# Performance work log

Hardware: AMD Instinct MI355X
Metric: run time of the kernel (lower is better)

## Reference

```python
import jax, jax.numpy as jnp
import numpy as np

N_FILTER = 64
IMAGE_SIZE = 64
CHANNELS = 3
N_CALLS = 16  # n_calls * 16 with n_calls=1
EPS = 1e-5


def _sobel_kernels(c):
    kx = jnp.array([[-1., 0., 1.], [-2., 0., 2.], [-1., 0., 1.]], jnp.float32) / 8.0
    ky = kx.T
    # depthwise OIHW kernels: (C, 1, 3, 3)
    return jnp.tile(kx[None, None], (c, 1, 1, 1)), jnp.tile(ky[None, None], (c, 1, 1, 1))


def _dwconv(x, k):
    return jax.lax.conv_general_dilated(
        x, k, window_strides=(1, 1), padding='SAME',
        feature_group_count=x.shape[1],
        dimension_numbers=('NCHW', 'OIHW', 'NCHW'))


def setup_inputs() -> dict:
    key = jax.random.key(0)
    k1, k2, k3 = jax.random.split(key, 3)
    B, L = 16, 512
    fin, fout = N_FILTER * 3, N_FILTER
    return {
        'lat': jax.random.normal(k1, (B, L), jnp.float32),
        'Wk': jax.random.normal(k2, (L, fin * fout), jnp.float32) * 0.02,
        'bk': jnp.zeros((fin * fout,), jnp.float32),
        'Wb': jax.random.normal(k3, (L, fout), jnp.float32) * 0.02,
        'bb': jnp.zeros((fout,), jnp.float32),
        'leak_factor': jnp.asarray(0.1, jnp.float32),
    }


def reference(lat, Wk, bk, Wb, bb, leak_factor):
    B = lat.shape[0]
    fin, fout = N_FILTER * 3, N_FILTER
    kx, ky = _sobel_kernels(N_FILTER)

    # seed: zeros with a 1.0 in channel 0 at the image center
    out0 = jnp.zeros((B, N_FILTER, IMAGE_SIZE, IMAGE_SIZE), jnp.float32)
    out0 = out0.at[:, 0, IMAGE_SIZE // 2, IMAGE_SIZE // 2].set(1.0)

    leak = jnp.clip(leak_factor, 0.001, 1000.0)

    # per-sample dynamic 1x1 conv weights/bias (constant across the loop)
    w = (lat @ Wk + bk).reshape(B, fout, fin)   # (B, fout, fin)
    b = (lat @ Wb + bb)                          # (B, fout)

    def step(out, _):
        # Sobel perception: [identity, grad_x, grad_y] -> (B, 3*nf, H, W)
        p = jnp.concatenate([out, _dwconv(out, kx), _dwconv(out, ky)], axis=1)
        # InstanceNorm2d (affine=False): normalize over H, W per sample/channel
        mu = p.mean(axis=(2, 3), keepdims=True)
        var = p.var(axis=(2, 3), keepdims=True)
        p = (p - mu) * jax.lax.rsqrt(var + EPS)
        # latent-conditioned dynamic 1x1 conv
        new = jnp.einsum('bchw,boc->bohw', p, w) + b[:, :, None, None]
        out = out + leak * new
        return out, out

    out, embs = jax.lax.scan(step, out0, None, length=N_CALLS)
    out_embs = jnp.concatenate([out0[None], embs], axis=0)  # (N_CALLS+1, B, nf, H, W)

    out_raw = out[:, :CHANNELS]
    return jnp.clip(out_raw, -1.0, 1.0), out_embs, out_raw
```

## Files before the change

### kernel.cpp

```cpp
#include <hip/hip_runtime.h>
#include <cstdint>
#include <cstddef>

#define NB 16
#define NC 64
#define HW 4096
#define SLICE ((size_t)(NB*NC*HW))
#define NSTEP 16

#define WS_WT    ((size_t)0)
#define WS_BV    ((size_t)196608)
#define WS_LATT  ((size_t)197632)
#define WS_SV    ((size_t)205824)
#define WS_SVMU  ((size_t)208896)

typedef _Float16 half8 __attribute__((ext_vector_type(8)));
typedef float f32x4 __attribute__((ext_vector_type(4)));

__global__ void k_latT(const float* __restrict__ lat, float* __restrict__ latT) {
  int t = threadIdx.x;
  for (int idx = t; idx < 16*512; idx += 256) {
    int b = idx >> 9, k = idx & 511;
    latT[k*16 + b] = lat[idx];
  }
}

__global__ __launch_bounds__(256) void k_w(const float* __restrict__ latT,
    const float* __restrict__ Wk, const float* __restrict__ bk,
    const float* __restrict__ Wb, const float* __restrict__ bb,
    float* __restrict__ wT, float* __restrict__ bvec) {
  int t = threadIdx.x;
  if (blockIdx.x < 48) {
    int j = blockIdx.x*256 + t;
    float acc[16];
#pragma unroll
    for (int b = 0; b < 16; b++) acc[b] = 0.f;
#pragma unroll 4
    for (int k = 0; k < 512; k++) {
      float wv = Wk[(size_t)k*12288 + j];
      const float* lt = (const float*)__builtin_assume_aligned(latT + k*16, 64);
#pragma unroll
      for (int b = 0; b < 16; b++) acc[b] = fmaf(lt[b], wv, acc[b]);
    }
    int o = j / 192, cf = j % 192;
    int g = cf >> 6, c = cf & 63;
    float bkj = bk[j];
#pragma unroll
    for (int b = 0; b < 16; b++)
      wT[(((size_t)(b*3 + g))*64 + o)*64 + c] = acc[b] + bkj;
  } else if (t < 64) {
    int j = t;
    float acc[16];
#pragma unroll
    for (int b = 0; b < 16; b++) acc[b] = 0.f;
    for (int k = 0; k < 512; k++) {
      float wv = Wb[k*64 + j];
      const float* lt = (const float*)__builtin_assume_aligned(latT + k*16, 64);
#pragma unroll
      for (int b = 0; b < 16; b++) acc[b] = fmaf(lt[b], wv, acc[b]);
    }
    float bbj = bb[j];
#pragma unroll
    for (int b = 0; b < 16; b++) bvec[b*64 + j] = acc[b] + bbj;
  }
}

__global__ void k_init(float* __restrict__ e0) {
  int idx4 = (blockIdx.x*256 + threadIdx.x) * 4;
  float4 v = make_float4(0.f, 0.f, 0.f, 0.f);
  if ((idx4 & 262143) == 2080) v.x = 1.0f;
  *(float4*)(e0 + idx4) = v;
}

__global__ __launch_bounds__(256) void k_stats(const float* __restrict__ st,
    float* __restrict__ svb, float* __restrict__ svmub) {
  int c = blockIdx.x, b = blockIdx.y, t = threadIdx.x;
  __shared__ float img[HW];
  __shared__ float red[4][6];
  const size_t chan = (size_t)(b*NC + c) * HW;
  const float4* src4 = (const float4*)(st + chan);
  float4* img4 = (float4*)img;
#pragma unroll
  for (int i = 0; i < 4; i++) img4[i*256 + t] = src4[i*256 + t];
  __syncthreads();

  int w = t & 63;
  int h0 = (t >> 6) * 16;
  bool wl = (w > 0), wr = (w < 63);
  float s0=0,q0=0,s1=0,q1=0,s2=0,q2=0;
  float d_prev=0.f, s_prev=0.f, d_cur, s_cur, v_cur;
  if (h0 > 0) {
    const float* row = img + (h0-1)*64;
    float xl = wl ? row[w-1] : 0.f;
    float xc = row[w];
    float xr = wr ? row[w+1] : 0.f;
    d_prev = xr - xl; s_prev = xl + 2.f*xc + xr;
  }
  {
    const float* row = img + h0*64;
    float xl = wl ? row[w-1] : 0.f;
    float xc = row[w];
    float xr = wr ? row[w+1] : 0.f;
    d_cur = xr - xl; s_cur = xl + 2.f*xc + xr; v_cur = xc;
  }
#pragma unroll
  for (int k = 0; k < 16; k++) {
    int hn = h0 + k + 1;
    float d_nxt=0.f, s_nxt=0.f, v_nxt=0.f;
    if (hn < 64) {
      const float* row = img + hn*64;
      float xl = wl ? row[w-1] : 0.f;
      float xc = row[w];
      float xr = wr ? row[w+1] : 0.f;
      d_nxt = xr - xl; s_nxt = xl + 2.f*xc + xr; v_nxt = xc;
    }
    float gx = (d_prev + 2.f*d_cur + d_nxt) * 0.125f;
    float gy = (s_nxt - s_prev) * 0.125f;
    float v = v_cur;
    s0 += v;  q0 = fmaf(v, v, q0);
    s1 += gx; q1 = fmaf(gx, gx, q1);
    s2 += gy; q2 = fmaf(gy, gy, q2);
    d_prev = d_cur; s_prev = s_cur;
    d_cur = d_nxt; s_cur = s_nxt; v_cur = v_nxt;
  }
#pragma unroll
  for (int off = 32; off >= 1; off >>= 1) {
    s0 += __shfl_xor(s0, off); q0 += __shfl_xor(q0, off);
    s1 += __shfl_xor(s1, off); q1 += __shfl_xor(q1, off);
    s2 += __shfl_xor(s2, off); q2 += __shfl_xor(q2, off);
  }
  int lane = t & 63, wv = t >> 6;
  if (lane == 0) {
    red[wv][0]=s0; red[wv][1]=q0; red[wv][2]=s1;
    red[wv][3]=q1; red[wv][4]=s2; red[wv][5]=q2;
  }
  __syncthreads();
  if (t == 0) {
    float r[6];
#pragma unroll
    for (int u = 0; u < 6; u++) r[u] = red[0][u]+red[1][u]+red[2][u]+red[3][u];
#pragma unroll
    for (int g = 0; g < 3; g++) {
      float mu  = r[2*g] * (1.f/HW);
      float var = fmaxf(r[2*g+1]*(1.f/HW) - mu*mu, 0.f);
      float sv  = 1.f / sqrtf(var + 1e-5f);
      svb  [b*192 + g*64 + c] = sv;
      svmub[b*192 + g*64 + c] = sv * mu;
    }
  }
}

struct SB {
  alignas(16) _Float16 Bhi[6144];
  alignas(16) _Float16 Blo[6144];
  alignas(16) _Float16 Whi[6144];
  alignas(16) _Float16 Wlo[6144];
  float svL[192], svmuL[192], biasL[192], bvecL[64];
};

__global__ __launch_bounds__(256, 2) void k_fused(const float* __restrict__ st,
    float* __restrict__ stn, const float* __restrict__ wT,
    const float* __restrict__ bvec, const float* __restrict__ svb,
    const float* __restrict__ svmub, const float* __restrict__ leakp,
    float* __restrict__ out0, float* __restrict__ out2, int last) {
  __shared__ SB sh;
  int bid = blockIdx.x, t = threadIdx.x;
  int b = bid >> 6;
  int r = (bid & 7) * 8 + ((bid >> 3) & 7);
  int lane = t & 63, wt = t >> 6;
  const float* stb = st + (size_t)b*NC*HW;
  float leak = fminf(fmaxf(leakp[0], 0.001f), 1000.f);

  if (t < 192) { sh.svL[t] = svb[b*192 + t]; sh.svmuL[t] = svmub[b*192 + t]; }
  if (t < 64) sh.bvecL[t] = bvec[b*64 + t];

  float biasacc = 0.f;
  f32x4 accA[4] = {}; f32x4 accB[12] = {}; f32x4 accC[12] = {};
  float xw0[3][8], xw1[3][8];

#define LOADW(KC, XW)                                                    \
  _Pragma("unroll")                                                      \
  for (int i = 0; i < 3; i++) {                                          \
    int u = t + i*256;                                                   \
    int c8 = u / 192, pxu = u % 192;                                     \
    int rho = pxu >> 6, ww = pxu & 63;                                   \
    int row = r - 1 + rho;                                               \
    bool ok = (row >= 0) && (row < 64);                                  \
    int rowc = ok ? row : 0;                                             \
    const float* gp = stb + (size_t)((KC)*32 + c8*8)*HW + rowc*64 + ww;  \
    _Pragma("unroll")                                                    \
    for (int ii = 0; ii < 8; ii++) {                                     \
      float val = gp[(size_t)ii*HW];                                     \
      XW[i][ii] = ok ? val : 0.f;                                        \
    }                                                                    \
  }

#define PACKW(XW)                                                        \
  _Pragma("unroll")                                                      \
  for (int i = 0; i < 3; i++) {                                          \
    int u = t + i*256;                                                   \
    int c8 = u / 192, pxu = u % 192;                                     \
    half8 hv, lv;                                                        \
    _Pragma("unroll")                                                    \
    for (int ii = 0; ii < 8; ii++) {                                     \
      float x = XW[i][ii];                                               \
      _Float16 h = (_Float16)x;                                          \
      hv[ii] = h;                                                        \
      lv[ii] = (_Float16)(x - (float)h);                                 \
    }                                                                    \
    int di = (c8*192 + (pxu ^ c8)) * 8;                                  \
    *(half8*)(sh.Bhi + di) = hv;                                         \
    *(half8*)(sh.Blo + di) = lv;                                         \
  }

#define WSTAGE(KC)                                                       \
  if (t < 192) {                                                         \
    int g = t >> 6, o = t & 63;                                          \
    const float* wrow = wT + (((size_t)(b*3 + g))*64 + o)*64 + (KC)*32;  \
    _Pragma("unroll")                                                    \
    for (int s = 0; s < 4; s++) {                                        \
      float4 va = *(const float4*)(wrow + s*8);                          \
      float4 vb4 = *(const float4*)(wrow + s*8 + 4);                     \
      float wv[8] = {va.x,va.y,va.z,va.w,vb4.x,vb4.y,vb4.z,vb4.w};       \
      half8 hv, lv;                                                      \
      _Pragma("unroll")                                                  \
      for (int jj = 0; jj < 8; jj++) {                                   \
        int cg = g*64 + (KC)*32 + s*8 + jj;                              \
        float scaled = wv[jj] * sh.svL[cg];                              \
        biasacc = fmaf(wv[jj], sh.svmuL[cg], biasacc);                   \
        _Float16 h = (_Float16)scaled;                                   \
        hv[jj] = h;                                                      \
        lv[jj] = (_Float16)(scaled - (float)h);                          \
      }                                                                  \
      int swz = (s ^ (o & 3) ^ ((o >> 2) & 3)) & 3;                      \
      int sidx = (g*64 + o)*32 + (swz << 3);                             \
      *(half8*)(sh.Whi + sidx) = hv;                                     \
      *(half8*)(sh.Wlo + sidx) = lv;                                     \
    }                                                                    \
  }

#define MFMAS()                                                          \
  {                                                                      \
    half8 ahi[3], alo[3];                                                \
    int oa = wt*16 + (lane & 15);                                        \
    int c4 = lane >> 4;                                                  \
    int slotx = (c4 ^ (oa & 3) ^ ((oa >> 2) & 3)) & 3;                   \
    _Pragma("unroll")                                                    \
    for (int g = 0; g < 3; g++) {                                        \
      int sidx = (g*64 + oa)*32 + (slotx << 3);                          \
      ahi[g] = *(const half8*)(sh.Whi + sidx);                           \
      alo[g] = *(const half8*)(sh.Wlo + sidx);                           \
    }                                                                    \
    _Pragma("unroll")                                                    \
    for (int n = 0; n < 12; n++) {                                       \
      int px = n*16 + (lane & 15);                                       \
      int bidx = (c4*192 + (px ^ c4))*8;                                 \
      half8 bh = *(const half8*)(sh.Bhi + bidx);                         \
      half8 bl = *(const half8*)(sh.Blo + bidx);                         \
      accB[n] = __builtin_amdgcn_mfma_f32_16x16x32_f16(ahi[1], bh, accB[n], 0,0,0); \
      accB[n] = __builtin_amdgcn_mfma_f32_16x16x32_f16(ahi[1], bl, accB[n], 0,0,0); \
      accB[n] = __builtin_amdgcn_mfma_f32_16x16x32_f16(alo[1], bh, accB[n], 0,0,0); \
      accC[n] = __builtin_amdgcn_mfma_f32_16x16x32_f16(ahi[2], bh, accC[n], 0,0,0); \
      accC[n] = __builtin_amdgcn_mfma_f32_16x16x32_f16(ahi[2], bl, accC[n], 0,0,0); \
      accC[n] = __builtin_amdgcn_mfma_f32_16x16x32_f16(alo[2], bh, accC[n], 0,0,0); \
      if (n >= 4 && n < 8) {                                             \
        accA[n-4] = __builtin_amdgcn_mfma_f32_16x16x32_f16(ahi[0], bh, accA[n-4], 0,0,0); \
        accA[n-4] = __builtin_amdgcn_mfma_f32_16x16x32_f16(ahi[0], bl, accA[n-4], 0,0,0); \
        accA[n-4] = __builtin_amdgcn_mfma_f32_16x16x32_f16(alo[0], bh, accA[n-4], 0,0,0); \
      }                                                                  \
    }                                                                    \
  }

  LOADW(0, xw0)
  __syncthreads();
  PACKW(xw0)
  WSTAGE(0)
  __syncthreads();
  LOADW(1, xw1)
  MFMAS()
  __syncthreads();
  PACKW(xw1)
  WSTAGE(1)
  __syncthreads();
  MFMAS()

  if (t < 192) sh.biasL[t] = biasacc;
  __syncthreads();

#pragma unroll
  for (int j = 0; j < 4; j++) {
    int o = wt*16 + ((lane >> 4) << 2) + j;
    float Sx[4], Sy[4];
#pragma unroll
    for (int nc = 0; nc < 4; nc++) {
      Sx[nc] = accB[nc][j] + 2.f*accB[4+nc][j] + accB[8+nc][j];
      Sy[nc] = accC[8+nc][j] - accC[nc][j];
    }
    float bt = sh.bvecL[o] - sh.biasL[o] - sh.biasL[64+o] - sh.biasL[128+o];
#pragma unroll
    for (int nc = 0; nc < 4; nc++) {
      int nm = (nc > 0) ? nc-1 : 0;
      int np = (nc < 3) ? nc+1 : 3;
      float xl1 = __shfl(Sx[nc], (lane - 1) & 63);
      float xl2 = (nc > 0) ? __shfl(Sx[nm], (lane + 15) & 63) : 0.f;
      float xL  = (lane & 15) ? xl1 : xl2;
      float xr1 = __shfl(Sx[nc], (lane + 1) & 63);
      float xr2 = (nc < 3) ? __shfl(Sx[np], (lane - 15) & 63) : 0.f;
      float xR  = ((lane & 15) == 15) ? xr2 : xr1;
      float yl1 = __shfl(Sy[nc], (lane - 1) & 63);
      float yl2 = (nc > 0) ? __shfl(Sy[nm], (lane + 15) & 63) : 0.f;
      float yL  = (lane & 15) ? yl1 : yl2;
      float yr1 = __shfl(Sy[nc], (lane + 1) & 63);
      float yr2 = (nc < 3) ? __shfl(Sy[np], (lane - 15) & 63) : 0.f;
      float yR  = ((lane & 15) == 15) ? yr2 : yr1;
      float gx = (xR - xL) * 0.125f;
      float gy = (yL + 2.f*Sy[nc] + yR) * 0.125f;
      float nw = accA[nc][j] + gx + gy + bt;
      int wpx = nc*16 + (lane & 15);
      size_t gi = (size_t)(b*NC + o)*HW + (size_t)r*64 + wpx;
      float nv = st[gi] + leak * nw;
      stn[gi] = nv;
      if (last && o < 3) {
        size_t oi = (size_t)(b*3 + o)*HW + (size_t)r*64 + wpx;
        out2[oi] = nv;
        out0[oi] = fminf(fmaxf(nv, -1.f), 1.f);
      }
    }
  }
#undef LOADW
#undef PACKW
#undef WSTAGE
#undef MFMAS
}

extern "C" void kernel_launch(void* const* d_in, const int* in_sizes, int n_in,
                              void* d_out, int out_size, void* d_ws, size_t ws_size,
                              hipStream_t stream) {
  const float* lat   = (const float*)d_in[0];
  const float* Wk    = (const float*)d_in[1];
  const float* bk    = (const float*)d_in[2];
  const float* Wb    = (const float*)d_in[3];
  const float* bb    = (const float*)d_in[4];
  const float* leakp = (const float*)d_in[5];
  float* out = (float*)d_out;
  float* ws  = (float*)d_ws;
  float* wT    = ws + WS_WT;
  float* bvec  = ws + WS_BV;
  float* latT  = ws + WS_LATT;
  float* svbuf = ws + WS_SV;
  float* svmub = ws + WS_SVMU;
  float* out0 = out;
  float* embs = out + 196608;
  float* out2 = out + 196608 + 17*SLICE;

  hipLaunchKernelGGL(k_latT, dim3(1),    dim3(256), 0, stream, lat, latT);
  hipLaunchKernelGGL(k_w,    dim3(49),   dim3(256), 0, stream, latT, Wk, bk, Wb, bb, wT, bvec);
  hipLaunchKernelGGL(k_init, dim3(4096), dim3(256), 0, stream, embs);
  for (int tstep = 0; tstep < NSTEP; tstep++) {
    const float* stc = embs + (size_t)tstep*SLICE;
    float*       stn = embs + (size_t)(tstep+1)*SLICE;
    hipLaunchKernelGGL(k_stats, dim3(64,16), dim3(256), 0, stream, stc, svbuf, svmub);
    hipLaunchKernelGGL(k_fused, dim3(1024), dim3(256), 0, stream,
                       stc, stn, wT, bvec, svbuf, svmub, leakp,
                       out0, out2, (int)(tstep == NSTEP-1));
  }
}
```

Measured before the change: 599.9 us.

## Process two rows per fused block to reuse staged weights; shuffle-based stats stencil

The fused step kernel now handles two image rows per block, with half as many blocks. The per-sample weight scaling, fp16 hi/lo split and bias reduction are staged once into a double-sized shared buffer and reused for both rows instead of being redone per row. The stats kernel drops its shared-memory image copy and builds horizontal neighbours with wavefront shuffles, reading rows directly from global memory. The trade-off is larger shared memory per block and half the grid parallelism (512 blocks), which may lower occupancy and leave less latency hiding.

Result: no change. 599.8 us (-0.0%).

```diff
diff --git a/kernel.cpp b/kernel.cpp
--- a/kernel.cpp
+++ b/kernel.cpp
@@ -75,61 +75,54 @@
 __global__ __launch_bounds__(256) void k_stats(const float* __restrict__ st,
     float* __restrict__ svb, float* __restrict__ svmub) {
   int c = blockIdx.x, b = blockIdx.y, t = threadIdx.x;
-  __shared__ float img[HW];
   __shared__ float red[4][6];
-  const size_t chan = (size_t)(b*NC + c) * HW;
-  const float4* src4 = (const float4*)(st + chan);
-  float4* img4 = (float4*)img;
-#pragma unroll
-  for (int i = 0; i < 4; i++) img4[i*256 + t] = src4[i*256 + t];
-  __syncthreads();
-
-  int w = t & 63;
-  int h0 = (t >> 6) * 16;
-  bool wl = (w > 0), wr = (w < 63);
+  const float* base = st + (size_t)(b*NC + c) * HW;
+  int w = t & 63, wv = t >> 6, h0 = wv * 16;
   float s0=0,q0=0,s1=0,q1=0,s2=0,q2=0;
+
   float d_prev=0.f, s_prev=0.f, d_cur, s_cur, v_cur;
+#define MKDS(X, D, S)                                  \
+  {                                                    \
+    float xl = __shfl((X), (w + 63) & 63);             \
+    float xr = __shfl((X), (w + 1) & 63);              \
+    if (w == 0)  xl = 0.f;                             \
+    if (w == 63) xr = 0.f;                             \
+    (D) = xr - xl; (S) = xl + 2.f*(X) + xr;            \
+  }
   if (h0 > 0) {
-    const float* row = img + (h0-1)*64;
-    float xl = wl ? row[w-1] : 0.f;
-    float xc = row[w];
-    float xr = wr ? row[w+1] : 0.f;
-    d_prev = xr - xl; s_prev = xl + 2.f*xc + xr;
+    float x = base[(h0-1)*64 + w];
+    MKDS(x, d_prev, s_prev)
   }
   {
-    const float* row = img + h0*64;
-    float xl = wl ? row[w-1] : 0.f;
-    float xc = row[w];
-    float xr = wr ? row[w+1] : 0.f;
-    d_cur = xr - xl; s_cur = xl + 2.f*xc + xr; v_cur = xc;
+    float x = base[h0*64 + w];
+    MKDS(x, d_cur, s_cur)
+    v_cur = x;
   }
 #pragma unroll
   for (int k = 0; k < 16; k++) {
     int hn = h0 + k + 1;
     float d_nxt=0.f, s_nxt=0.f, v_nxt=0.f;
     if (hn < 64) {
-      const float* row = img + hn*64;
-      float xl = wl ? row[w-1] : 0.f;
-      float xc = row[w];
-      float xr = wr ? row[w+1] : 0.f;
-      d_nxt = xr - xl; s_nxt = xl + 2.f*xc + xr; v_nxt = xc;
+      float x = base[hn*64 + w];
+      MKDS(x, d_nxt, s_nxt)
+      v_nxt = x;
     }
     float gx = (d_prev + 2.f*d_cur + d_nxt) * 0.125f;
     float gy = (s_nxt - s_prev) * 0.125f;
-    float v = v_cur;
-    s0 += v;  q0 = fmaf(v, v, q0);
-    s1 += gx; q1 = fmaf(gx, gx, q1);
-    s2 += gy; q2 = fmaf(gy, gy, q2);
+    s0 += v_cur; q0 = fmaf(v_cur, v_cur, q0);
+    s1 += gx;    q1 = fmaf(gx, gx, q1);
+    s2 += gy;    q2 = fmaf(gy, gy, q2);
     d_prev = d_cur; s_prev = s_cur;
     d_cur = d_nxt; s_cur = s_nxt; v_cur = v_nxt;
   }
+#undef MKDS
 #pragma unroll
   for (int off = 32; off >= 1; off >>= 1) {
     s0 += __shfl_xor(s0, off); q0 += __shfl_xor(q0, off);
     s1 += __shfl_xor(s1, off); q1 += __shfl_xor(q1, off);
     s2 += __shfl_xor(s2, off); q2 += __shfl_xor(q2, off);
   }
-  int lane = t & 63, wv = t >> 6;
+  int lane = t & 63;
   if (lane == 0) {
     red[wv][0]=s0; red[wv][1]=q0; red[wv][2]=s1;
     red[wv][3]=q1; red[wv][4]=s2; red[wv][5]=q2;
@@ -150,11 +143,11 @@
   }
 }
 
-struct SB {
+struct SB2 {
   alignas(16) _Float16 Bhi[6144];
   alignas(16) _Float16 Blo[6144];
-  alignas(16) _Float16 Whi[6144];
-  alignas(16) _Float16 Wlo[6144];
+  alignas(16) _Float16 Whi[2][6144];
+  alignas(16) _Float16 Wlo[2][6144];
   float svL[192], svmuL[192], biasL[192], bvecL[64];
 };
 
@@ -163,28 +156,55 @@
     const float* __restrict__ bvec, const float* __restrict__ svb,
     const float* __restrict__ svmub, const float* __restrict__ leakp,
     float* __restrict__ out0, float* __restrict__ out2, int last) {
-  __shared__ SB sh;
+  __shared__ SB2 sh;
   int bid = blockIdx.x, t = threadIdx.x;
-  int b = bid >> 6;
-  int r = (bid & 7) * 8 + ((bid >> 3) & 7);
+  int b = bid >> 5;
+  int r0 = (bid & 7) * 8 + ((bid >> 3) & 3) * 2;
   int lane = t & 63, wt = t >> 6;
   const float* stb = st + (size_t)b*NC*HW;
   float leak = fminf(fmaxf(leakp[0], 0.001f), 1000.f);
 
   if (t < 192) { sh.svL[t] = svb[b*192 + t]; sh.svmuL[t] = svmub[b*192 + t]; }
   if (t < 64) sh.bvecL[t] = bvec[b*64 + t];
-
-  float biasacc = 0.f;
-  f32x4 accA[4] = {}; f32x4 accB[12] = {}; f32x4 accC[12] = {};
-  float xw0[3][8], xw1[3][8];
-
-#define LOADW(KC, XW)                                                    \
+  __syncthreads();
+
+  if (t < 192) {
+    int g = t >> 6, o = t & 63;
+    float biasacc = 0.f;
+#pragma unroll
+    for (int kc = 0; kc < 2; kc++) {
+      const float* wrow = wT + (((size_t)(b*3 + g))*64 + o)*64 + kc*32;
+#pragma unroll
+      for (int s = 0; s < 4; s++) {
+        float4 va = *(const float4*)(wrow + s*8);
+        float4 vb4 = *(const float4*)(wrow + s*8 + 4);
+        float wv[8] = {va.x,va.y,va.z,va.w,vb4.x,vb4.y,vb4.z,vb4.w};
+        half8 hv, lv;
+#pragma unroll
+        for (int jj = 0; jj < 8; jj++) {
+          int cg = g*64 + kc*32 + s*8 + jj;
+          float scaled = wv[jj] * sh.svL[cg];
+          biasacc = fmaf(wv[jj], sh.svmuL[cg], biasacc);
+          _Float16 h = (_Float16)scaled;
+          hv[jj] = h;
+          lv[jj] = (_Float16)(scaled - (float)h);
+        }
+        int swz = (s ^ (o & 3) ^ ((o >> 2) & 3)) & 3;
+        int sidx = (g*64 + o)*32 + (swz << 3);
+        *(half8*)(&sh.Whi[kc][sidx]) = hv;
+        *(half8*)(&sh.Wlo[kc][sidx]) = lv;
+      }
+    }
+    sh.biasL[t] = biasacc;
+  }
+
+#define LOADW(KC, R, XW)                                                 \
   _Pragma("unroll")                                                      \
   for (int i = 0; i < 3; i++) {                                          \
     int u = t + i*256;                                                   \
     int c8 = u / 192, pxu = u % 192;                                     \
     int rho = pxu >> 6, ww = pxu & 63;                                   \
-    int row = r - 1 + rho;                                               \
+    int row = (R) - 1 + rho;                                             \
     bool ok = (row >= 0) && (row < 64);                                  \
     int rowc = ok ? row : 0;                                             \
     const float* gp = stb + (size_t)((KC)*32 + c8*8)*HW + rowc*64 + ww;  \
@@ -213,33 +233,7 @@
     *(half8*)(sh.Blo + di) = lv;                                         \
   }
 
-#define WSTAGE(KC)                                                       \
-  if (t < 192) {                                                         \
-    int g = t >> 6, o = t & 63;                                          \
-    const float* wrow = wT + (((size_t)(b*3 + g))*64 + o)*64 + (KC)*32;  \
-    _Pragma("unroll")                                                    \
-    for (int s = 0; s < 4; s++) {                                        \
-      float4 va = *(const float4*)(wrow + s*8);                          \
-      float4 vb4 = *(const float4*)(wrow + s*8 + 4);                     \
-      float wv[8] = {va.x,va.y,va.z,va.w,vb4.x,vb4.y,vb4.z,vb4.w};       \
-      half8 hv, lv;                                                      \
-      _Pragma("unroll")                                                  \
-      for (int jj = 0; jj < 8; jj++) {                                   \
-        int cg = g*64 + (KC)*32 + s*8 + jj;                              \
-        float scaled = wv[jj] * sh.svL[cg];                              \
-        biasacc = fmaf(wv[jj], sh.svmuL[cg], biasacc);                   \
-        _Float16 h = (_Float16)scaled;                                   \
-        hv[jj] = h;                                                      \
-        lv[jj] = (_Float16)(scaled - (float)h);                          \
-      }                                                                  \
-      int swz = (s ^ (o & 3) ^ ((o >> 2) & 3)) & 3;                      \
-      int sidx = (g*64 + o)*32 + (swz << 3);                             \
-      *(half8*)(sh.Whi + sidx) = hv;                                     \
-      *(half8*)(sh.Wlo + sidx) = lv;                                     \
-    }                                                                    \
-  }
-
-#define MFMAS()                                                          \
+#define MFMAS(KC)                                                        \
   {                                                                      \
     half8 ahi[3], alo[3];                                                \
     int oa = wt*16 + (lane & 15);                                        \
@@ -248,8 +242,8 @@
     _Pragma("unroll")                                                    \
     for (int g = 0; g < 3; g++) {                                        \
       int sidx = (g*64 + oa)*32 + (slotx << 3);                          \
-      ahi[g] = *(const half8*)(sh.Whi + sidx);                           \
-      alo[g] = *(const half8*)(sh.Wlo + sidx);                           \
+      ahi[g] = *(const half8*)(&sh.Whi[KC][sidx]);                       \
+      alo[g] = *(const half8*)(&sh.Wlo[KC][sidx]);                       \
     }                                                                    \
     _Pragma("unroll")                                                    \
     for (int n = 0; n < 12; n++) {                                       \
@@ -271,65 +265,66 @@
     }                                                                    \
   }
 
-  LOADW(0, xw0)
-  __syncthreads();
-  PACKW(xw0)
-  WSTAGE(0)
-  __syncthreads();
-  LOADW(1, xw1)
-  MFMAS()
-  __syncthreads();
-  PACKW(xw1)
-  WSTAGE(1)
-  __syncthreads();
-  MFMAS()
-
-  if (t < 192) sh.biasL[t] = biasacc;
-  __syncthreads();
-
-#pragma unroll
-  for (int j = 0; j < 4; j++) {
-    int o = wt*16 + ((lane >> 4) << 2) + j;
-    float Sx[4], Sy[4];
-#pragma unroll
-    for (int nc = 0; nc < 4; nc++) {
-      Sx[nc] = accB[nc][j] + 2.f*accB[4+nc][j] + accB[8+nc][j];
-      Sy[nc] = accC[8+nc][j] - accC[nc][j];
-    }
-    float bt = sh.bvecL[o] - sh.biasL[o] - sh.biasL[64+o] - sh.biasL[128+o];
-#pragma unroll
-    for (int nc = 0; nc < 4; nc++) {
-      int nm = (nc > 0) ? nc-1 : 0;
-      int np = (nc < 3) ? nc+1 : 3;
-      float xl1 = __shfl(Sx[nc], (lane - 1) & 63);
-      float xl2 = (nc > 0) ? __shfl(Sx[nm], (lane + 15) & 63) : 0.f;
-      float xL  = (lane & 15) ? xl1 : xl2;
-      float xr1 = __shfl(Sx[nc], (lane + 1) & 63);
-      float xr2 = (nc < 3) ? __shfl(Sx[np], (lane - 15) & 63) : 0.f;
-      float xR  = ((lane & 15) == 15) ? xr2 : xr1;
-      float yl1 = __shfl(Sy[nc], (lane - 1) & 63);
-      float yl2 = (nc > 0) ? __shfl(Sy[nm], (lane + 15) & 63) : 0.f;
-      float yL  = (lane & 15) ? yl1 : yl2;
-      float yr1 = __shfl(Sy[nc], (lane + 1) & 63);
-      float yr2 = (nc < 3) ? __shfl(Sy[np], (lane - 15) & 63) : 0.f;
-      float yR  = ((lane & 15) == 15) ? yr2 : yr1;
-      float gx = (xR - xL) * 0.125f;
-      float gy = (yL + 2.f*Sy[nc] + yR) * 0.125f;
-      float nw = accA[nc][j] + gx + gy + bt;
-      int wpx = nc*16 + (lane & 15);
-      size_t gi = (size_t)(b*NC + o)*HW + (size_t)r*64 + wpx;
-      float nv = st[gi] + leak * nw;
-      stn[gi] = nv;
-      if (last && o < 3) {
-        size_t oi = (size_t)(b*3 + o)*HW + (size_t)r*64 + wpx;
-        out2[oi] = nv;
-        out0[oi] = fminf(fmaxf(nv, -1.f), 1.f);
+#pragma unroll
+  for (int rr = 0; rr < 2; rr++) {
+    int r = r0 + rr;
+    f32x4 accA[4] = {}; f32x4 accB[12] = {}; f32x4 accC[12] = {};
+    float xw0[3][8], xw1[3][8];
+
+    LOADW(0, r, xw0)
+    __syncthreads();
+    PACKW(xw0)
+    __syncthreads();
+    LOADW(1, r, xw1)
+    MFMAS(0)
+    __syncthreads();
+    PACKW(xw1)
+    __syncthreads();
+    MFMAS(1)
+
+#pragma unroll
+    for (int j = 0; j < 4; j++) {
+      int o = wt*16 + ((lane >> 4) << 2) + j;
+      float Sx[4], Sy[4];
+#pragma unroll
+      for (int nc = 0; nc < 4; nc++) {
+        Sx[nc] = accB[nc][j] + 2.f*accB[4+nc][j] + accB[8+nc][j];
+        Sy[nc] = accC[8+nc][j] - accC[nc][j];
+      }
+      float bt = sh.bvecL[o] - sh.biasL[o] - sh.biasL[64+o] - sh.biasL[128+o];
+#pragma unroll
+      for (int nc = 0; nc < 4; nc++) {
+        int nm = (nc > 0) ? nc-1 : 0;
+        int np = (nc < 3) ? nc+1 : 3;
+        float xl1 = __shfl(Sx[nc], (lane - 1) & 63);
+        float xl2 = (nc > 0) ? __shfl(Sx[nm], (lane + 15) & 63) : 0.f;
+        float xL  = (lane & 15) ? xl1 : xl2;
+        float xr1 = __shfl(Sx[nc], (lane + 1) & 63);
+        float xr2 = (nc < 3) ? __shfl(Sx[np], (lane - 15) & 63) : 0.f;
+        float xR  = ((lane & 15) == 15) ? xr2 : xr1;
+        float yl1 = __shfl(Sy[nc], (lane - 1) & 63);
+        float yl2 = (nc > 0) ? __shfl(Sy[nm], (lane + 15) & 63) : 0.f;
+        float yL  = (lane & 15) ? yl1 : yl2;
+        float yr1 = __shfl(Sy[nc], (lane + 1) & 63);
+        float yr2 = (nc < 3) ? __shfl(Sy[np], (lane - 15) & 63) : 0.f;
+        float yR  = ((lane & 15) == 15) ? yr2 : yr1;
+        float gx = (xR - xL) * 0.125f;
+        float gy = (yL + 2.f*Sy[nc] + yR) * 0.125f;
+        float nw = accA[nc][j] + gx + gy + bt;
+        int wpx = nc*16 + (lane & 15);
+        size_t gi = (size_t)(b*NC + o)*HW + (size_t)r*64 + wpx;
+        float nv = st[gi] + leak * nw;
+        stn[gi] = nv;
+        if (last && o < 3) {
+          size_t oi = (size_t)(b*3 + o)*HW + (size_t)r*64 + wpx;
+          out2[oi] = nv;
+          out0[oi] = fminf(fmaxf(nv, -1.f), 1.f);
+        }
       }
     }
   }
 #undef LOADW
 #undef PACKW
-#undef WSTAGE
 #undef MFMAS
 }
 
@@ -360,7 +355,7 @@
     const float* stc = embs + (size_t)tstep*SLICE;
     float*       stn = embs + (size_t)(tstep+1)*SLICE;
     hipLaunchKernelGGL(k_stats, dim3(64,16), dim3(256), 0, stream, stc, svbuf, svmub);
-    hipLaunchKernelGGL(k_fused, dim3(1024), dim3(256), 0, stream,
+    hipLaunchKernelGGL(k_fused, dim3(512), dim3(256), 0, stream,
                        stc, stn, wT, bvec, svbuf, svmub, leakp,
                        out0, out2, (int)(tstep == NSTEP-1));
   }
```
